# Performance work log

Measured on AMD Instinct MI355X. Metric: run time of the kernel, lower is better.

The kernel has to match this reference:

```python
import jax, jax.numpy as jnp
import numpy as np

B, T, D = 2, 2048, 2048
N, KH, H = 16, 8, 128  # query heads, kv heads, head_dim
S = 2048               # cache size
EPS = 1e-6
ROPE_THETA = 1000000.0
K_MASK = -0.7 * float(np.finfo(np.float32).max)  # jax _get_large_negative(float32)


def _rms_norm(x, w):
    rms = jnp.sqrt(jnp.mean(x.astype(jnp.float32) ** 2, axis=-1, keepdims=True) + EPS)
    return (w * x / rms).astype(x.dtype)


def _rope_embeddings(positions, head_dim):
    fraction = jnp.arange(0, head_dim, 2, dtype=jnp.float32) / head_dim
    inv_freq = 1.0 / (ROPE_THETA ** fraction)
    sinusoid = jnp.einsum('BT,k->BTk', positions.astype(jnp.float32), inv_freq,
                          precision=jax.lax.Precision.HIGHEST)
    return jnp.sin(sinusoid), jnp.cos(sinusoid)


def _apply_rope(x, sin, cos):
    h = x.shape[-1] // 2
    x1, x2 = x[..., :h], x[..., h:]
    s, c = sin[:, :, None, :], cos[:, :, None, :]
    return jnp.concatenate([x1 * c - x2 * s, x2 * c + x1 * s], axis=-1).astype(x.dtype)


def _positions_from_segment_ids(seg):
    t = seg.shape[1]
    pos = jnp.arange(t, dtype=jnp.int32)[None, :] - jnp.argmax(seg, axis=1)[:, None]
    return jnp.where(seg != 0, pos, 2 ** 30)


def _num_left_pad(seg):
    return jnp.sum(jnp.cumsum(seg != 0, axis=-1) == 0, axis=-1).astype(jnp.int32)


def _attention(x, q_w, k_w, v_w, o_w, q_norm_w, k_norm_w, k_cache, v_cache,
               segment_ids, start_ind, cur_ind):
    b, t, _ = x.shape
    s = k_cache.shape[1]
    n, kh, h = q_w.shape[1], k_w.shape[1], q_w.shape[2]

    q = _rms_norm(jnp.einsum('BTD,DNH->BTNH', x, q_w), q_norm_w)  # [B,T,N,H]
    k = _rms_norm(jnp.einsum('BSD,DKH->BSKH', x, k_w), k_norm_w)  # [B,T,K,H]
    v = jnp.einsum('BSD,DKH->BSKH', x, v_w)                       # [B,T,K,H]

    start = jnp.where(start_ind < 0, _num_left_pad(segment_ids), start_ind)
    pos = _positions_from_segment_ids(segment_ids) + cur_ind
    sin, cos = _rope_embeddings(pos, h)
    q = _apply_rope(q, sin, cos)
    k = _apply_rope(k, sin, cos)

    # KV-cache update at cur_ind
    k_cache = jax.lax.dynamic_update_slice(k_cache, k, (0, cur_ind, 0, 0))
    v_cache = jax.lax.dynamic_update_slice(v_cache, v, (0, cur_ind, 0, 0))

    # GQA: group query heads per kv head
    qg = q.reshape(b, t, kh, n // kh, h)
    logits = jnp.einsum('BTHGD,BSHD->BHGTS', qg, k_cache) * (h ** -0.5)

    q_pos = cur_ind + jnp.arange(t, dtype=jnp.int32)[None, :] - start[:, None]  # [B,T]
    ts = jnp.arange(s, dtype=jnp.int32)
    kv_seg = (ts[None, :] >= start[:, None]) & (ts[None, :] < cur_ind + t)      # [B,S] bool
    k_pos = ts[None, :] - start[:, None]                                        # [B,S]
    causal = k_pos[:, None, :] <= q_pos[:, :, None]                             # [B,T,S]
    # faithful to original: bool kv segment ids compared against int segment_ids
    seg_mask = kv_seg[:, None, :].astype(segment_ids.dtype) == segment_ids[:, :, None]
    final_mask = (causal & seg_mask)[:, None, None, :, :]                       # [B,1,1,T,S]

    logits = jnp.where(final_mask, logits, K_MASK)
    attn = jax.nn.softmax(logits.astype(jnp.float32), axis=-1).astype(logits.dtype)
    o = jnp.einsum('BHGTS,BSHD->BTHGD', attn, v_cache).reshape(b, t, n, h)
    return jnp.einsum('BTNH,NHD->BTD', o, o_w)


def setup_inputs() -> dict:
    key = jax.random.key(0)
    ks = jax.random.split(key, 5)
    scale = 0.02
    return {
        'x': jax.random.normal(ks[0], (B, T, D), jnp.float32),
        'q_w': jax.random.normal(ks[1], (D, N, H), jnp.float32) * scale,
        'k_w': jax.random.normal(ks[2], (D, KH, H), jnp.float32) * scale,
        'v_w': jax.random.normal(ks[3], (D, KH, H), jnp.float32) * scale,
        'o_w': jax.random.normal(ks[4], (N, H, D), jnp.float32) * scale,
        'q_norm_w': jnp.ones((H,), jnp.float32),
        'k_norm_w': jnp.ones((H,), jnp.float32),
        'k_cache': jnp.zeros((B, S, KH, H), jnp.float32),
        'v_cache': jnp.zeros((B, S, KH, H), jnp.float32),
        'segment_ids': jnp.ones((B, T), jnp.int32),
        'start_ind': jnp.zeros((B,), jnp.int32),
        'cur_ind': 0,
        'right_pads': 0,
    }


def reference(x, q_w, k_w, v_w, o_w, q_norm_w, k_norm_w, k_cache, v_cache,
              segment_ids, start_ind, cur_ind, right_pads):
    # right_pads only advances the cache write pointer (stateful side effect); it
    # does not affect the attention output.
    return _attention(x, q_w, k_w, v_w, o_w, q_norm_w, k_norm_w,
                      k_cache, v_cache, segment_ids, start_ind, cur_ind)
```

## Files before the change

kernel.cpp:

```cpp
#include <hip/hip_runtime.h>
#include <hip/hip_fp16.h>
#include <climits>
#include <math.h>

#define Bc   2
#define Tc   2048
#define Dc   2048
#define Nc   16
#define KHc  8
#define Hc   128
#define Sc   2048

constexpr float EPSc   = 1e-6f;
constexpr float SCALE2 = 0.1275174477984469f;

typedef short short8 __attribute__((ext_vector_type(8)));
typedef _Float16 half8 __attribute__((ext_vector_type(8)));
typedef __fp16 fp16x2 __attribute__((ext_vector_type(2)));
typedef float float4v __attribute__((ext_vector_type(4)));

union U16x8 { uint4 u; short8 s8; half8 h8; unsigned short us[8]; };
union H2U  { fp16x2 h; unsigned u; };
union S8H8 { short8 s; half8 h; };

__device__ __forceinline__ unsigned short f2bf(float f) {
    union { float f; unsigned u; } v; v.f = f;
    unsigned r = v.u + 0x7FFFu + ((v.u >> 16) & 1u);
    return (unsigned short)(r >> 16);
}
__device__ __forceinline__ float bf2f(unsigned short u) {
    union { unsigned u; float f; } v; v.u = ((unsigned)u) << 16;
    return v.f;
}

__device__ __forceinline__ void tc_body(const float* __restrict__ in,
                                        unsigned short* __restrict__ out,
                                        int R, int C, int bx, int by, int tid,
                                        float tile[32][33])
{
    int c0 = bx * 32, r0 = by * 32;
#pragma unroll
    for (int i = 0; i < 4; ++i) {
        int row = (tid >> 5) + i * 8, col = tid & 31;
        tile[row][col] = in[(size_t)(r0 + row) * C + c0 + col];
    }
    __syncthreads();
#pragma unroll
    for (int i = 0; i < 4; ++i) {
        int rowo = (tid >> 5) + i * 8, colo = tid & 31;
        out[(size_t)(c0 + rowo) * R + r0 + colo] = f2bf(tile[colo][rowo]);
    }
}

__global__ __launch_bounds__(256) void prep(const float* __restrict__ x,
                                            const float* __restrict__ qw,
                                            const float* __restrict__ kw,
                                            const float* __restrict__ vw,
                                            const float* __restrict__ ow,
                                            const int* __restrict__ seg,
                                            const int* __restrict__ start_ind,
                                            int* __restrict__ meta,
                                            unsigned short* __restrict__ xb,
                                            unsigned short* __restrict__ qkvwT,
                                            unsigned short* __restrict__ owT)
{
    __shared__ float tile[32][33];
    __shared__ int s_max, s_amax, s_nz;
    int id = blockIdx.x;
    int tid = threadIdx.x;

    if (id < Bc) {
        int b = id;
        if (tid == 0) { s_max = INT_MIN; s_amax = Tc; s_nz = Tc; }
        __syncthreads();
        int lmax = INT_MIN;
        for (int t = tid; t < Tc; t += 256) lmax = max(lmax, seg[b * Tc + t]);
        atomicMax(&s_max, lmax);
        __syncthreads();
        int mv = s_max;
        int lamax = Tc, lnz = Tc;
        for (int t = tid; t < Tc; t += 256) {
            int v = seg[b * Tc + t];
            if (v == mv) lamax = min(lamax, t);
            if (v != 0)  lnz   = min(lnz, t);
        }
        atomicMin(&s_amax, lamax);
        atomicMin(&s_nz, lnz);
        __syncthreads();
        if (tid == 0) {
            meta[b] = s_amax;
            int st = start_ind[b];
            meta[Bc + b] = (st < 0) ? s_nz : st;
        }
        return;
    }
    id -= Bc;
    if (id < 4096) {
        size_t base = ((size_t)id * 256 + tid) * 8;
        float4 a = *(const float4*)&x[base];
        float4 b = *(const float4*)&x[base + 4];
        U16x8 o;
        o.us[0] = f2bf(a.x); o.us[1] = f2bf(a.y); o.us[2] = f2bf(a.z); o.us[3] = f2bf(a.w);
        o.us[4] = f2bf(b.x); o.us[5] = f2bf(b.y); o.us[6] = f2bf(b.z); o.us[7] = f2bf(b.w);
        *(uint4*)&xb[base] = o.u;
        return;
    }
    id -= 4096;
    if (id < 4096) { tc_body(qw, qkvwT, 2048, 2048, id & 63, id >> 6, tid, tile); return; }
    id -= 4096;
    if (id < 2048) { tc_body(kw, qkvwT + (size_t)2048 * 2048, 2048, 1024, id & 31, id >> 5, tid, tile); return; }
    id -= 2048;
    if (id < 2048) { tc_body(vw, qkvwT + (size_t)3072 * 2048, 2048, 1024, id & 31, id >> 5, tid, tile); return; }
    id -= 2048;
    tc_body(ow, owT, 2048, 2048, id & 63, id >> 6, tid, tile);
}

#define GSYNC_IN()  do { asm volatile("" ::: "memory"); \
                         __builtin_amdgcn_s_barrier(); \
                         asm volatile("s_waitcnt lgkmcnt(0)" ::: "memory"); \
                         __builtin_amdgcn_sched_barrier(0); \
                         __builtin_amdgcn_s_setprio(1); } while (0)
#define GSYNC_OUT() do { __builtin_amdgcn_s_setprio(0); \
                         __builtin_amdgcn_sched_barrier(0); \
                         asm volatile("" ::: "memory"); \
                         __builtin_amdgcn_s_barrier(); } while (0)
#define GSYNC_OUT_KT() do { __builtin_amdgcn_s_setprio(0); \
                         __builtin_amdgcn_sched_barrier(0); \
                         asm volatile("s_waitcnt vmcnt(4)" ::: "memory"); \
                         __builtin_amdgcn_s_barrier(); \
                         asm volatile("" ::: "memory"); } while (0)

__global__ __launch_bounds__(512, 2) void gemm256(const unsigned short* __restrict__ A,
                                                  const unsigned short* __restrict__ BT,
                                                  void* __restrict__ Cout,
                                                  int M, int N, int K, int out_fp32)
{
    __shared__ __align__(16) unsigned short As[2 * 16384];
    __shared__ __align__(16) unsigned short Bs[2 * 16384];

    int tid = threadIdx.x;
    int lane = tid & 63, w = tid >> 6;
    int quad = lane >> 4, l15 = lane & 15;

    int gx = gridDim.x;
    int nwg = gx * gridDim.y;
    int lin = blockIdx.y * gx + blockIdx.x;
    int swz = (lin & 7) * (nwg >> 3) + (lin >> 3);
    int bm = (swz / gx) * 256, bn = (swz % gx) * 256;

    int KT = K >> 6;

    int colswz = (((lane & 7) ^ ((lane >> 3) & 7)) << 3);
    int r0 = (w * 2) * 8 + (lane >> 3);
    int r1 = (w * 2 + 1) * 8 + (lane >> 3);
    const unsigned short* Ab0 = A + (size_t)(bm + r0) * K + colswz;
    const unsigned short* Ab1 = A + (size_t)(bm + r1) * K + colswz;
    const unsigned short* Bb0 = BT + (size_t)(bn + r0) * K + colswz;
    const unsigned short* Bb1 = BT + (size_t)(bn + r1) * K + colswz;
    size_t hK = (size_t)128 * K;

    unsigned short* dA0 = As + (w * 2) * 512;
    unsigned short* dA1 = As + (w * 2 + 1) * 512;
    unsigned short* dB0 = Bs + (w * 2) * 512;
    unsigned short* dB1 = Bs + (w * 2 + 1) * 512;

    auto stA = [&](int kt, int h, int bufp) __attribute__((always_inline)) {
        __builtin_amdgcn_global_load_lds(
            (__attribute__((address_space(1))) void*)(Ab0 + h * hK + (size_t)kt * 64),
            (__attribute__((address_space(3))) void*)(dA0 + bufp * 16384 + h * 8192), 16, 0, 0);
        __builtin_amdgcn_global_load_lds(
            (__attribute__((address_space(1))) void*)(Ab1 + h * hK + (size_t)kt * 64),
            (__attribute__((address_space(3))) void*)(dA1 + bufp * 16384 + h * 8192), 16, 0, 0);
    };
    auto stB = [&](int kt, int h, int bufp) __attribute__((always_inline)) {
        __builtin_amdgcn_global_load_lds(
            (__attribute__((address_space(1))) void*)(Bb0 + h * hK + (size_t)kt * 64),
            (__attribute__((address_space(3))) void*)(dB0 + bufp * 16384 + h * 8192), 16, 0, 0);
        __builtin_amdgcn_global_load_lds(
            (__attribute__((address_space(1))) void*)(Bb1 + h * hK + (size_t)kt * 64),
            (__attribute__((address_space(3))) void*)(dB1 + bufp * 16384 + h * 8192), 16, 0, 0);
    };

    int ards = (w >> 2) * 8192;
    int brds = (w & 3) * 4096;
    int rowb = l15 * 64;
    int swA = l15 & 7;
    int cof0 = ((quad) ^ swA) << 3;
    int cof1 = ((4 + quad) ^ swA) << 3;

    float4v acc[8][4];
#pragma unroll
    for (int i = 0; i < 8; ++i)
#pragma unroll
        for (int j = 0; j < 4; ++j) acc[i][j] = (float4v)0.f;

    stA(0, 0, 0); stA(0, 1, 0); stB(0, 0, 0); stB(0, 1, 0);
    stA(1, 0, 1); stA(1, 1, 1);
    asm volatile("s_waitcnt vmcnt(4)" ::: "memory");
    __builtin_amdgcn_s_barrier();
    asm volatile("" ::: "memory");

    auto ktile = [&](int kt, int bufp) __attribute__((always_inline)) {
        bool sB = (kt + 1) < KT;
        bool sA = (kt + 2) < KT;
        const unsigned short* ab = As + bufp * 16384 + ards + rowb;
        const unsigned short* bb = Bs + bufp * 16384 + brds + rowb;
        short8 afl[2][4], afh[2][4], bfa[2][2], bfb[2][2];

#pragma unroll
        for (int mi = 0; mi < 4; ++mi) {
            afl[0][mi] = *(const short8*)&ab[mi * 1024 + cof0];
            afl[1][mi] = *(const short8*)&ab[mi * 1024 + cof1];
        }
#pragma unroll
        for (int ni = 0; ni < 2; ++ni) {
            bfa[0][ni] = *(const short8*)&bb[ni * 1024 + cof0];
            bfa[1][ni] = *(const short8*)&bb[ni * 1024 + cof1];
        }
        if (sB) stB(kt + 1, 0, bufp ^ 1);
        GSYNC_IN();
#pragma unroll
        for (int kk = 0; kk < 2; ++kk)
#pragma unroll
            for (int mi = 0; mi < 4; ++mi)
#pragma unroll
                for (int ni = 0; ni < 2; ++ni)
                    acc[mi][ni] = __builtin_amdgcn_mfma_f32_16x16x32_bf16(afl[kk][mi], bfa[kk][ni], acc[mi][ni], 0, 0, 0);
        GSYNC_OUT();

#pragma unroll
        for (int mi = 0; mi < 4; ++mi) {
            afh[0][mi] = *(const short8*)&ab[(4 + mi) * 1024 + cof0];
            afh[1][mi] = *(const short8*)&ab[(4 + mi) * 1024 + cof1];
        }
#pragma unroll
        for (int ni = 0; ni < 2; ++ni) {
            bfb[0][ni] = *(const short8*)&bb[(2 + ni) * 1024 + cof0];
            bfb[1][ni] = *(const short8*)&bb[(2 + ni) * 1024 + cof1];
        }
        if (sB) stB(kt + 1, 1, bufp ^ 1);
        GSYNC_IN();
#pragma unroll
        for (int kk = 0; kk < 2; ++kk)
#pragma unroll
            for (int mi = 0; mi < 4; ++mi)
#pragma unroll
                for (int ni = 0; ni < 2; ++ni)
                    acc[mi][2 + ni] = __builtin_amdgcn_mfma_f32_16x16x32_bf16(afl[kk][mi], bfb[kk][ni], acc[mi][2 + ni], 0, 0, 0);
        GSYNC_OUT();

#pragma unroll
        for (int ni = 0; ni < 2; ++ni) {
            bfa[0][ni] = *(const short8*)&bb[ni * 1024 + cof0];
            bfa[1][ni] = *(const short8*)&bb[ni * 1024 + cof1];
        }
        if (sA) stA(kt + 2, 0, bufp);
        GSYNC_IN();
#pragma unroll
        for (int kk = 0; kk < 2; ++kk)
#pragma unroll
            for (int mi = 0; mi < 4; ++mi)
#pragma unroll
                for (int ni = 0; ni < 2; ++ni)
                    acc[4 + mi][ni] = __builtin_amdgcn_mfma_f32_16x16x32_bf16(afh[kk][mi], bfa[kk][ni], acc[4 + mi][ni], 0, 0, 0);
        GSYNC_OUT();

#pragma unroll
        for (int ni = 0; ni < 2; ++ni) {
            bfb[0][ni] = *(const short8*)&bb[(2 + ni) * 1024 + cof0];
            bfb[1][ni] = *(const short8*)&bb[(2 + ni) * 1024 + cof1];
        }
        if (sA) stA(kt + 2, 1, bufp);
        GSYNC_IN();
#pragma unroll
        for (int kk = 0; kk < 2; ++kk)
#pragma unroll
            for (int mi = 0; mi < 4; ++mi)
#pragma unroll
                for (int ni = 0; ni < 2; ++ni)
                    acc[4 + mi][2 + ni] = __builtin_amdgcn_mfma_f32_16x16x32_bf16(afh[kk][mi], bfb[kk][ni], acc[4 + mi][2 + ni], 0, 0, 0);
        GSYNC_OUT_KT();
    };

    for (int kt = 0; kt < KT; kt += 2) {
        ktile(kt, 0);
        ktile(kt + 1, 1);
    }

    int wm = (w >> 2) * 128, wn = (w & 3) * 64;
#pragma unroll
    for (int mi = 0; mi < 8; ++mi)
#pragma unroll
        for (int ni = 0; ni < 4; ++ni)
#pragma unroll
            for (int reg = 0; reg < 4; ++reg) {
                int row = bm + wm + mi * 16 + quad * 4 + reg;
                int col = bn + wn + ni * 16 + l15;
                float v = acc[mi][ni][reg];
                if (out_fp32) ((float*)Cout)[(size_t)row * N + col] = v;
                else ((unsigned short*)Cout)[(size_t)row * N + col] = f2bf(v);
            }
}

__global__ __launch_bounds__(256) void post(unsigned short* __restrict__ QKVh,
                                            unsigned short* __restrict__ Kall,
                                            unsigned short* __restrict__ Vt,
                                            const float* __restrict__ qw,
                                            const float* __restrict__ kw,
                                            const int* __restrict__ seg,
                                            const int* __restrict__ meta,
                                            const int* __restrict__ cur_ptr,
                                            const float* __restrict__ kc,
                                            const float* __restrict__ vc)
{
    int id = blockIdx.x;
    int tid = threadIdx.x;
    int cur = cur_ptr[0];

    if (id < 24576) {
        int rowid = id * 4 + (tid >> 6);
        int lane = tid & 63;
        int hh = rowid % 24;
        int bt = rowid / 24;
        int t = bt & (Tc - 1);
        int b = bt >> 11;

        const unsigned short* in;
        unsigned short* out;
        const float* wt;
        if (hh < 16) {
            unsigned short* p = QKVh + (size_t)bt * 4096 + hh * Hc;
            in = p; out = p; wt = qw;
        } else {
            int kh = hh - 16;
            in = QKVh + (size_t)bt * 4096 + 2048 + kh * Hc;
            out = Kall + (((size_t)b * Sc + cur + t) * KHc + kh) * Hc;
            wt = kw;
        }
        float v1 = bf2f(in[lane]), v2 = bf2f(in[lane + 64]);
        float ssq = v1 * v1 + v2 * v2;
#pragma unroll
        for (int off = 1; off < 64; off <<= 1) ssq += __shfl_xor(ssq, off);
        float rinv = rsqrtf(ssq * (1.0f / Hc) + EPSc);

        int sg = seg[bt];
        long long pos = (sg != 0) ? (long long)(t - meta[b]) : (long long)(1 << 30);
        float posf = (float)(pos + (long long)cur);
        float inv_freq = exp2f(-(float)lane * (19.931568569324174f / 64.0f));
        float s, c;
        sincosf(posf * inv_freq, &s, &c);

        float n1 = wt[lane] * v1 * rinv;
        float n2 = wt[lane + 64] * v2 * rinv;
        out[lane]      = f2bf(n1 * c - n2 * s);
        out[lane + 64] = f2bf(n2 * c + n1 * s);
        return;
    }
    id -= 24576;
    if (id < 2048) {
        size_t base = ((size_t)id * 256 + tid) * 8;
        int s = (int)((base >> 10) & (Sc - 1));
        if (s >= cur && s < cur + Tc) return;
        float4 a = *(const float4*)&kc[base];
        float4 b = *(const float4*)&kc[base + 4];
        U16x8 o;
        o.us[0] = f2bf(a.x); o.us[1] = f2bf(a.y); o.us[2] = f2bf(a.z); o.us[3] = f2bf(a.w);
        o.us[4] = f2bf(b.x); o.us[5] = f2bf(b.y); o.us[6] = f2bf(b.z); o.us[7] = f2bf(b.w);
        *(uint4*)&Kall[base] = o.u;
        return;
    }
    id -= 2048;
    {
        int gid = id * 256 + tid;
        int h  = gid & 127;
        int s8 = ((gid >> 7) & 255) * 8;
        int kh = (gid >> 15) & 7;
        int b  = gid >> 18;
        int curT = cur + Tc;
        unsigned short tmp[8];
#pragma unroll
        for (int e = 0; e < 8; ++e) {
            int s = s8 + e;
            float f;
            if (s >= cur && s < curT)
                f = bf2f(QKVh[(size_t)(b * Tc + (s - cur)) * 4096 + 3072 + kh * Hc + h]);
            else
                f = vc[((size_t)(b * Sc + s) * KHc + kh) * Hc + h];
            tmp[e] = __half_as_ushort(__float2half(f));
        }
        *(uint4*)&Vt[(((size_t)b * KHc + kh) * Hc + h) * Sc + s8] = *(uint4*)tmp;
    }
}

__global__ __launch_bounds__(512, 4) void flash_mfma(const unsigned short* __restrict__ Qb,
                                                     const unsigned short* __restrict__ Kall,
                                                     const unsigned short* __restrict__ Vt,
                                                     const int* __restrict__ seg,
                                                     const int* __restrict__ meta,
                                                     const int* __restrict__ cur_ptr,
                                                     unsigned short* __restrict__ Ob)
{
    __shared__ __align__(16) unsigned short Ks[64 * 128];
    __shared__ __align__(16) unsigned short Vs[128 * 64];
    __shared__ __align__(16) unsigned short Ps[128 * 64];

    int tid = threadIdx.x;
    int lane = tid & 63, w = tid >> 6;
    int quad = lane >> 4, l15 = lane & 15;
    int bid = blockIdx.x;
    int raw = bid & 15;
    int n  = (bid >> 4) & 15;
    int b  = bid >> 8;
    int qt = (b == 0) ? raw : (15 - raw);
    int kh = n >> 1;
    int cur = cur_ptr[0];
    int startb = meta[Bc + b];
    int curT = cur + Tc;
    int t0 = qt * 128 + w * 16;

    short8 qf[4];
#pragma unroll
    for (int ks = 0; ks < 4; ++ks) {
        int row = t0 + l15;
        U16x8 uq;
        uq.u = *(const uint4*)&Qb[(size_t)(b * Tc + row) * 4096 + n * Hc + ks * 32 + quad * 8];
        qf[ks] = uq.s8;
    }

    int trow0 = t0 + l15;
    int sg0 = seg[b * Tc + trow0];
    int cls = (sg0 == 0) ? 0 : ((sg0 == 1) ? 1 : 2);
    int ct  = cur + trow0;
    unsigned long long mball = __ballot(cls == 1);
    bool allseg1 = (mball == 0xFFFFFFFFFFFFFFFFull);

    float lsum = 0.f;
    float4v oT[8];
#pragma unroll
    for (int i = 0; i < 8; ++i) oT[i] = (float4v)0.f;

    int s_end = min(Sc, cur + qt * 128 + 128);
    int nch = (s_end + 63) >> 6;

    const size_t kstride = (size_t)KHc * Hc;
    const unsigned short* kptr[2];
    unsigned short* kdst[2];
#pragma unroll
    for (int i = 0; i < 2; ++i) {
        int j = w * 2 + i;
        int row = j * 4 + (lane >> 4);
        int pl = lane & 15;
        int pg = pl ^ ((row >> 1) & 7);
        kptr[i] = Kall + (size_t)b * Sc * kstride + (size_t)row * kstride + kh * Hc + pg * 8;
        kdst[i] = Ks + j * 512;
    }
    const unsigned short* vptr[2];
    unsigned short* vdst[2];
#pragma unroll
    for (int i = 0; i < 2; ++i) {
        int j = w * 2 + i;
        int h = j * 8 + (lane >> 3);
        int pl = lane & 7;
        int pg = pl ^ ((h >> 1) & 7);
        vptr[i] = Vt + ((size_t)b * KHc + kh) * (size_t)Hc * Sc + (size_t)h * Sc + pg * 8;
        vdst[i] = Vs + j * 512;
    }
    int sw3 = (l15 >> 1) & 7;
    int sw8 = l15 & 7;
    unsigned short* psrow = Ps + (w * 16 + l15) * 64;

    for (int c = 0; c < nch; ++c) {
        int s0 = c * 64;
#pragma unroll
        for (int i = 0; i < 2; ++i) {
            __builtin_amdgcn_global_load_lds(
                (__attribute__((address_space(1))) void*)(kptr[i] + (size_t)s0 * kstride),
                (__attribute__((address_space(3))) void*)kdst[i], 16, 0, 0);
            __builtin_amdgcn_global_load_lds(
                (__attribute__((address_space(1))) void*)(vptr[i] + s0),
                (__attribute__((address_space(3))) void*)vdst[i], 16, 0, 0);
        }
        __syncthreads();

        float4v st[4];
#pragma unroll
        for (int i = 0; i < 4; ++i) st[i] = (float4v)0.f;
        __builtin_amdgcn_s_setprio(1);
#pragma unroll
        for (int ks = 0; ks < 4; ++ks) {
#pragma unroll
            for (int stile = 0; stile < 4; ++stile) {
                short8 kf = *(const short8*)&Ks[(stile * 16 + l15) * 128 + ((ks * 4 + quad) ^ sw3) * 8];
                st[stile] = __builtin_amdgcn_mfma_f32_16x16x32_bf16(kf, qf[ks], st[stile], 0, 0, 0);
            }
        }
        __builtin_amdgcn_s_setprio(0);

        bool fullok = allseg1 && (s0 >= startb) && (s0 + 63 <= cur + t0) && (s0 + 63 < curT);

#pragma unroll
        for (int stile = 0; stile < 4; ++stile) {
            float p0, p1, p2, p3;
            if (fullok) {
                p0 = exp2f(st[stile][0] * SCALE2);
                p1 = exp2f(st[stile][1] * SCALE2);
                p2 = exp2f(st[stile][2] * SCALE2);
                p3 = exp2f(st[stile][3] * SCALE2);
            } else {
                float pp[4];
#pragma unroll
                for (int reg = 0; reg < 4; ++reg) {
                    int s = s0 + stile * 16 + quad * 4 + reg;
                    int kvseg = (s >= startb && s < curT) ? 1 : 0;
                    bool ok = (s <= ct) && (cls == kvseg);
                    pp[reg] = exp2f(ok ? st[stile][reg] * SCALE2 : -1e30f);
                }
                p0 = pp[0]; p1 = pp[1]; p2 = pp[2]; p3 = pp[3];
            }
            lsum += (p0 + p1) + (p2 + p3);
            H2U a, d;
            a.h = __builtin_amdgcn_cvt_pkrtz(p0, p1);
            d.h = __builtin_amdgcn_cvt_pkrtz(p2, p3);
            uint2 pk; pk.x = a.u; pk.y = d.u;
            *(uint2*)&psrow[(((stile * 2 + (quad >> 1)) ^ sw8) << 3) + (quad & 1) * 4] = pk;
        }

        __builtin_amdgcn_s_setprio(1);
#pragma unroll
        for (int kk = 0; kk < 2; ++kk) {
            S8H8 pf;
            pf.s = *(const short8*)&psrow[((kk * 4 + quad) ^ sw8) << 3];
#pragma unroll
            for (int htile = 0; htile < 8; ++htile) {
                S8H8 vf;
                vf.s = *(const short8*)&Vs[(htile * 16 + l15) * 64 + ((kk * 4 + quad) ^ sw3) * 8];
                oT[htile] = __builtin_amdgcn_mfma_f32_16x16x32_f16(vf.h, pf.h, oT[htile], 0, 0, 0);
            }
        }
        __builtin_amdgcn_s_setprio(0);

        __syncthreads();
    }

    float l = lsum;
    l += __shfl_xor(l, 16);
    l += __shfl_xor(l, 32);
    float linv = (l > 0.f) ? (1.0f / l) : 0.f;

    {
        int trow = t0 + l15;
        size_t base = ((size_t)(b * Tc + trow) * Nc + n) * Hc;
#pragma unroll
        for (int htile = 0; htile < 8; ++htile) {
            float4v v = oT[htile];
            unsigned short r0 = f2bf(v[0] * linv);
            unsigned short r1 = f2bf(v[1] * linv);
            unsigned short r2 = f2bf(v[2] * linv);
            unsigned short r3 = f2bf(v[3] * linv);
            uint2 pk;
            pk.x = (unsigned)r0 | ((unsigned)r1 << 16);
            pk.y = (unsigned)r2 | ((unsigned)r3 << 16);
            *(uint2*)&Ob[base + htile * 16 + quad * 4] = pk;
        }
    }
}

extern "C" void kernel_launch(void* const* d_in, const int* in_sizes, int n_in,
                              void* d_out, int out_size, void* d_ws, size_t ws_size,
                              hipStream_t stream)
{
    const float* x        = (const float*)d_in[0];
    const float* q_w      = (const float*)d_in[1];
    const float* k_w      = (const float*)d_in[2];
    const float* v_w      = (const float*)d_in[3];
    const float* o_w      = (const float*)d_in[4];
    const float* q_norm_w = (const float*)d_in[5];
    const float* k_norm_w = (const float*)d_in[6];
    const float* k_cache  = (const float*)d_in[7];
    const float* v_cache  = (const float*)d_in[8];
    const int*   seg      = (const int*)d_in[9];
    const int*   startind = (const int*)d_in[10];
    const int*   cur_ptr  = (const int*)d_in[11];
    (void)in_sizes; (void)n_in; (void)out_size; (void)ws_size;

    char* base = (char*)d_ws;
    int* meta = (int*)base;
    unsigned short* QKVh = (unsigned short*)(base + 1024);
    unsigned short* Kall = (unsigned short*)(base + 33555456);
    unsigned short* Vt   = (unsigned short*)(base + 41944064);
    unsigned short* xb   = (unsigned short*)(base + 50332672);
    unsigned short* qkvwT= (unsigned short*)(base + 67109888);
    unsigned short* owT  = (unsigned short*)(base + 83887104);
    unsigned short* Ob   = xb;

    prep<<<Bc + 4096 + 4096 + 2048 + 2048 + 4096, 256, 0, stream>>>(
        x, q_w, k_w, v_w, o_w, seg, startind, meta, xb, qkvwT, owT);

    gemm256<<<dim3(16, 16), 512, 0, stream>>>(xb, qkvwT, QKVh, Bc * Tc, 4096, Dc, 0);

    post<<<24576 + 2048 + 2048, 256, 0, stream>>>(QKVh, Kall, Vt,
        q_norm_w, k_norm_w, seg, meta, cur_ptr, k_cache, v_cache);

    flash_mfma<<<Bc * Nc * (Tc / 128), 512, 0, stream>>>(QKVh, Kall, Vt, seg, meta, cur_ptr, Ob);

    gemm256<<<dim3(8, 16), 512, 0, stream>>>(Ob, owT, d_out, Bc * Tc, Dc, Nc * Hc, 1);
}
```

Measured before the change: 393.0 us.

## Restructure GEMM k-loop to two barriers per tile with prefetch two ahead

Replaces the four-phase ping-pong schedule, which had a barrier pair around each MFMA quarter, with a two-phase loop. All A and B fragments are read from LDS up front, and half the MFMAs run before a single barrier. Global loads for tile kt+2 are then issued into the just-freed buffer and overlap the remaining MFMAs, with a vmcnt wait and barrier at the end. This removes barrier and sync overhead per k-tile but raises register pressure from holding all fragments at once and changes the load/compute interleaving.

```diff
diff --git a/kernel.cpp b/kernel.cpp
--- a/kernel.cpp
+++ b/kernel.cpp
@@ -115,21 +115,6 @@
     tc_body(ow, owT, 2048, 2048, id & 63, id >> 6, tid, tile);
 }
 
-#define GSYNC_IN()  do { asm volatile("" ::: "memory"); \
-                         __builtin_amdgcn_s_barrier(); \
-                         asm volatile("s_waitcnt lgkmcnt(0)" ::: "memory"); \
-                         __builtin_amdgcn_sched_barrier(0); \
-                         __builtin_amdgcn_s_setprio(1); } while (0)
-#define GSYNC_OUT() do { __builtin_amdgcn_s_setprio(0); \
-                         __builtin_amdgcn_sched_barrier(0); \
-                         asm volatile("" ::: "memory"); \
-                         __builtin_amdgcn_s_barrier(); } while (0)
-#define GSYNC_OUT_KT() do { __builtin_amdgcn_s_setprio(0); \
-                         __builtin_amdgcn_sched_barrier(0); \
-                         asm volatile("s_waitcnt vmcnt(4)" ::: "memory"); \
-                         __builtin_amdgcn_s_barrier(); \
-                         asm volatile("" ::: "memory"); } while (0)
-
 __global__ __launch_bounds__(512, 2) void gemm256(const unsigned short* __restrict__ A,
                                                   const unsigned short* __restrict__ BT,
                                                   void* __restrict__ Cout,
@@ -195,14 +180,12 @@
         for (int j = 0; j < 4; ++j) acc[i][j] = (float4v)0.f;
 
     stA(0, 0, 0); stA(0, 1, 0); stB(0, 0, 0); stB(0, 1, 0);
-    stA(1, 0, 1); stA(1, 1, 1);
-    asm volatile("s_waitcnt vmcnt(4)" ::: "memory");
+    stA(1, 0, 1); stA(1, 1, 1); stB(1, 0, 1); stB(1, 1, 1);
+    asm volatile("s_waitcnt vmcnt(8)" ::: "memory");
     __builtin_amdgcn_s_barrier();
     asm volatile("" ::: "memory");
 
     auto ktile = [&](int kt, int bufp) __attribute__((always_inline)) {
-        bool sB = (kt + 1) < KT;
-        bool sA = (kt + 2) < KT;
         const unsigned short* ab = As + bufp * 16384 + ards + rowb;
         const unsigned short* bb = Bs + bufp * 16384 + brds + rowb;
         short8 afl[2][4], afh[2][4], bfa[2][2], bfb[2][2];
@@ -217,29 +200,24 @@
             bfa[0][ni] = *(const short8*)&bb[ni * 1024 + cof0];
             bfa[1][ni] = *(const short8*)&bb[ni * 1024 + cof1];
         }
-        if (sB) stB(kt + 1, 0, bufp ^ 1);
-        GSYNC_IN();
-#pragma unroll
-        for (int kk = 0; kk < 2; ++kk)
-#pragma unroll
-            for (int mi = 0; mi < 4; ++mi)
-#pragma unroll
-                for (int ni = 0; ni < 2; ++ni)
-                    acc[mi][ni] = __builtin_amdgcn_mfma_f32_16x16x32_bf16(afl[kk][mi], bfa[kk][ni], acc[mi][ni], 0, 0, 0);
-        GSYNC_OUT();
-
+#pragma unroll
+        for (int ni = 0; ni < 2; ++ni) {
+            bfb[0][ni] = *(const short8*)&bb[(2 + ni) * 1024 + cof0];
+            bfb[1][ni] = *(const short8*)&bb[(2 + ni) * 1024 + cof1];
+        }
 #pragma unroll
         for (int mi = 0; mi < 4; ++mi) {
             afh[0][mi] = *(const short8*)&ab[(4 + mi) * 1024 + cof0];
             afh[1][mi] = *(const short8*)&ab[(4 + mi) * 1024 + cof1];
         }
-#pragma unroll
-        for (int ni = 0; ni < 2; ++ni) {
-            bfb[0][ni] = *(const short8*)&bb[(2 + ni) * 1024 + cof0];
-            bfb[1][ni] = *(const short8*)&bb[(2 + ni) * 1024 + cof1];
-        }
-        if (sB) stB(kt + 1, 1, bufp ^ 1);
-        GSYNC_IN();
+        __builtin_amdgcn_s_setprio(1);
+#pragma unroll
+        for (int kk = 0; kk < 2; ++kk)
+#pragma unroll
+            for (int mi = 0; mi < 4; ++mi)
+#pragma unroll
+                for (int ni = 0; ni < 2; ++ni)
+                    acc[mi][ni] = __builtin_amdgcn_mfma_f32_16x16x32_bf16(afl[kk][mi], bfa[kk][ni], acc[mi][ni], 0, 0, 0);
 #pragma unroll
         for (int kk = 0; kk < 2; ++kk)
 #pragma unroll
@@ -247,15 +225,18 @@
 #pragma unroll
                 for (int ni = 0; ni < 2; ++ni)
                     acc[mi][2 + ni] = __builtin_amdgcn_mfma_f32_16x16x32_bf16(afl[kk][mi], bfb[kk][ni], acc[mi][2 + ni], 0, 0, 0);
-        GSYNC_OUT();
-
-#pragma unroll
-        for (int ni = 0; ni < 2; ++ni) {
-            bfa[0][ni] = *(const short8*)&bb[ni * 1024 + cof0];
-            bfa[1][ni] = *(const short8*)&bb[ni * 1024 + cof1];
-        }
-        if (sA) stA(kt + 2, 0, bufp);
-        GSYNC_IN();
+        __builtin_amdgcn_s_setprio(0);
+        asm volatile("s_waitcnt lgkmcnt(0)" ::: "memory");
+        __builtin_amdgcn_sched_barrier(0);
+        __builtin_amdgcn_s_barrier();
+        asm volatile("" ::: "memory");
+
+        bool sA = (kt + 2) < KT;
+        if (sA) {
+            stA(kt + 2, 0, bufp); stA(kt + 2, 1, bufp);
+            stB(kt + 2, 0, bufp); stB(kt + 2, 1, bufp);
+        }
+        __builtin_amdgcn_s_setprio(1);
 #pragma unroll
         for (int kk = 0; kk < 2; ++kk)
 #pragma unroll
@@ -263,15 +244,6 @@
 #pragma unroll
                 for (int ni = 0; ni < 2; ++ni)
                     acc[4 + mi][ni] = __builtin_amdgcn_mfma_f32_16x16x32_bf16(afh[kk][mi], bfa[kk][ni], acc[4 + mi][ni], 0, 0, 0);
-        GSYNC_OUT();
-
-#pragma unroll
-        for (int ni = 0; ni < 2; ++ni) {
-            bfb[0][ni] = *(const short8*)&bb[(2 + ni) * 1024 + cof0];
-            bfb[1][ni] = *(const short8*)&bb[(2 + ni) * 1024 + cof1];
-        }
-        if (sA) stA(kt + 2, 1, bufp);
-        GSYNC_IN();
 #pragma unroll
         for (int kk = 0; kk < 2; ++kk)
 #pragma unroll
@@ -279,7 +251,12 @@
 #pragma unroll
                 for (int ni = 0; ni < 2; ++ni)
                     acc[4 + mi][2 + ni] = __builtin_amdgcn_mfma_f32_16x16x32_bf16(afh[kk][mi], bfb[kk][ni], acc[4 + mi][2 + ni], 0, 0, 0);
-        GSYNC_OUT_KT();
+        __builtin_amdgcn_s_setprio(0);
+        if (sA) asm volatile("s_waitcnt vmcnt(8)" ::: "memory");
+        else    asm volatile("s_waitcnt vmcnt(0)" ::: "memory");
+        __builtin_amdgcn_sched_barrier(0);
+        __builtin_amdgcn_s_barrier();
+        asm volatile("" ::: "memory");
     };
 
     for (int kt = 0; kt < KT; kt += 2) {
```

New measurement: 457.8 us. 1.16x slower.

## Add 128x128 tiled GEMM for output projection and vectorize weight transpose

Applied to the files above, without the earlier changes.

Adds a new gemm128 kernel (256 threads, 128x128 tiles, double-buffered LDS via global_load_lds) and uses it for the output projection. The previous 256x256 tiling launched only 128 workgroups, and the smaller tile raises that to 512 so more of the GPU's compute units stay busy. The prep transpose is also changed to use float4 loads and 16-byte packed bf16 stores, cutting the number of memory transactions. The trade-off is lower data reuse per tile and more total global traffic for the GEMM.

```diff
diff --git a/kernel.cpp b/kernel.cpp
--- a/kernel.cpp
+++ b/kernel.cpp
@@ -39,16 +39,21 @@
                                         float tile[32][33])
 {
     int c0 = bx * 32, r0 = by * 32;
-#pragma unroll
-    for (int i = 0; i < 4; ++i) {
-        int row = (tid >> 5) + i * 8, col = tid & 31;
-        tile[row][col] = in[(size_t)(r0 + row) * C + c0 + col];
+    {
+        int row = tid >> 3, col = (tid & 7) * 4;
+        float4 v = *(const float4*)&in[(size_t)(r0 + row) * C + c0 + col];
+        tile[row][col]     = v.x;
+        tile[row][col + 1] = v.y;
+        tile[row][col + 2] = v.z;
+        tile[row][col + 3] = v.w;
     }
     __syncthreads();
-#pragma unroll
-    for (int i = 0; i < 4; ++i) {
-        int rowo = (tid >> 5) + i * 8, colo = tid & 31;
-        out[(size_t)(c0 + rowo) * R + r0 + colo] = f2bf(tile[colo][rowo]);
+    if (tid < 128) {
+        int rowo = tid >> 2, s8 = (tid & 3) * 8;
+        U16x8 o;
+#pragma unroll
+        for (int k = 0; k < 8; ++k) o.us[k] = f2bf(tile[s8 + k][rowo]);
+        *(uint4*)&out[(size_t)(c0 + rowo) * R + r0 + s8] = o.u;
     }
 }
 
@@ -290,6 +295,136 @@
     int wm = (w >> 2) * 128, wn = (w & 3) * 64;
 #pragma unroll
     for (int mi = 0; mi < 8; ++mi)
+#pragma unroll
+        for (int ni = 0; ni < 4; ++ni)
+#pragma unroll
+            for (int reg = 0; reg < 4; ++reg) {
+                int row = bm + wm + mi * 16 + quad * 4 + reg;
+                int col = bn + wn + ni * 16 + l15;
+                float v = acc[mi][ni][reg];
+                if (out_fp32) ((float*)Cout)[(size_t)row * N + col] = v;
+                else ((unsigned short*)Cout)[(size_t)row * N + col] = f2bf(v);
+            }
+}
+
+__global__ __launch_bounds__(256, 2) void gemm128(const unsigned short* __restrict__ A,
+                                                  const unsigned short* __restrict__ BT,
+                                                  void* __restrict__ Cout,
+                                                  int M, int N, int K, int out_fp32)
+{
+    __shared__ __align__(16) unsigned short As[2 * 8192];
+    __shared__ __align__(16) unsigned short Bs[2 * 8192];
+
+    int tid = threadIdx.x;
+    int lane = tid & 63, w = tid >> 6;
+    int quad = lane >> 4, l15 = lane & 15;
+
+    int gx = gridDim.x;
+    int nwg = gx * gridDim.y;
+    int lin = blockIdx.y * gx + blockIdx.x;
+    int swz = (lin & 7) * (nwg >> 3) + (lin >> 3);
+    int bm = (swz / gx) * 128, bn = (swz % gx) * 128;
+
+    int KT = K >> 6;
+
+    int colswz = (((lane & 7) ^ ((lane >> 3) & 7)) << 3);
+    int r0 = w * 32 + (lane >> 3);
+    const unsigned short* Ab = A + (size_t)(bm + r0) * K + colswz;
+    const unsigned short* Bb = BT + (size_t)(bn + r0) * K + colswz;
+    size_t rowK8 = (size_t)8 * K;
+
+    unsigned short* dA = As + w * 2048;
+    unsigned short* dB = Bs + w * 2048;
+
+    auto stA = [&](int kt, int bufp) __attribute__((always_inline)) {
+#pragma unroll
+        for (int i = 0; i < 4; ++i)
+            __builtin_amdgcn_global_load_lds(
+                (__attribute__((address_space(1))) void*)(Ab + (size_t)i * rowK8 + (size_t)kt * 64),
+                (__attribute__((address_space(3))) void*)(dA + bufp * 8192 + i * 512), 16, 0, 0);
+    };
+    auto stB = [&](int kt, int bufp) __attribute__((always_inline)) {
+#pragma unroll
+        for (int i = 0; i < 4; ++i)
+            __builtin_amdgcn_global_load_lds(
+                (__attribute__((address_space(1))) void*)(Bb + (size_t)i * rowK8 + (size_t)kt * 64),
+                (__attribute__((address_space(3))) void*)(dB + bufp * 8192 + i * 512), 16, 0, 0);
+    };
+
+    int wm = (w >> 1) * 64, wn = (w & 1) * 64;
+    int swk = l15 & 7;
+    int cof0 = ((quad) ^ swk) << 3;
+    int cof1 = ((4 + quad) ^ swk) << 3;
+    const int arow = (wm + l15) * 64;
+    const int brow = (wn + l15) * 64;
+
+    float4v acc[4][4];
+#pragma unroll
+    for (int i = 0; i < 4; ++i)
+#pragma unroll
+        for (int j = 0; j < 4; ++j) acc[i][j] = (float4v)0.f;
+
+    stA(0, 0); stB(0, 0);
+    stA(1, 1);
+    asm volatile("s_waitcnt vmcnt(4)" ::: "memory");
+    __builtin_amdgcn_s_barrier();
+    asm volatile("" ::: "memory");
+
+    auto ktile = [&](int kt, int bufp) __attribute__((always_inline)) {
+        const unsigned short* ab = As + bufp * 8192 + arow;
+        const unsigned short* bb = Bs + bufp * 8192 + brow;
+        short8 af[2][4], bf[2][4];
+
+        if (kt + 1 < KT) stB(kt + 1, bufp ^ 1);
+#pragma unroll
+        for (int mi = 0; mi < 4; ++mi) {
+            af[0][mi] = *(const short8*)&ab[mi * 1024 + cof0];
+            af[1][mi] = *(const short8*)&ab[mi * 1024 + cof1];
+        }
+#pragma unroll
+        for (int ni = 0; ni < 4; ++ni) {
+            bf[0][ni] = *(const short8*)&bb[ni * 1024 + cof0];
+            bf[1][ni] = *(const short8*)&bb[ni * 1024 + cof1];
+        }
+        __builtin_amdgcn_s_setprio(1);
+#pragma unroll
+        for (int kk = 0; kk < 2; ++kk)
+#pragma unroll
+            for (int mi = 0; mi < 4; ++mi)
+#pragma unroll
+                for (int ni = 0; ni < 2; ++ni)
+                    acc[mi][ni] = __builtin_amdgcn_mfma_f32_16x16x32_bf16(af[kk][mi], bf[kk][ni], acc[mi][ni], 0, 0, 0);
+        __builtin_amdgcn_s_setprio(0);
+        asm volatile("s_waitcnt lgkmcnt(0)" ::: "memory");
+        __builtin_amdgcn_sched_barrier(0);
+        __builtin_amdgcn_s_barrier();
+        asm volatile("" ::: "memory");
+
+        bool sA = (kt + 2) < KT;
+        if (sA) stA(kt + 2, bufp);
+        __builtin_amdgcn_s_setprio(1);
+#pragma unroll
+        for (int kk = 0; kk < 2; ++kk)
+#pragma unroll
+            for (int mi = 0; mi < 4; ++mi)
+#pragma unroll
+                for (int ni = 2; ni < 4; ++ni)
+                    acc[mi][ni] = __builtin_amdgcn_mfma_f32_16x16x32_bf16(af[kk][mi], bf[kk][ni], acc[mi][ni], 0, 0, 0);
+        __builtin_amdgcn_s_setprio(0);
+        if (sA) asm volatile("s_waitcnt vmcnt(4)" ::: "memory");
+        else    asm volatile("s_waitcnt vmcnt(0)" ::: "memory");
+        __builtin_amdgcn_sched_barrier(0);
+        __builtin_amdgcn_s_barrier();
+        asm volatile("" ::: "memory");
+    };
+
+    for (int kt = 0; kt < KT; kt += 2) {
+        ktile(kt, 0);
+        ktile(kt + 1, 1);
+    }
+
+#pragma unroll
+    for (int mi = 0; mi < 4; ++mi)
 #pragma unroll
         for (int ni = 0; ni < 4; ++ni)
 #pragma unroll
@@ -603,5 +738,5 @@
 
     flash_mfma<<<Bc * Nc * (Tc / 128), 512, 0, stream>>>(QKVh, Kall, Vt, seg, meta, cur_ptr, Ob);
 
-    gemm256<<<dim3(8, 16), 512, 0, stream>>>(Ob, owT, d_out, Bc * Tc, Dc, Nc * Hc, 1);
-}
+    gemm128<<<dim3(16, 32), 256, 0, stream>>>(Ob, owT, d_out, Bc * Tc, Dc, Nc * Hc, 1);
+}
```

Result: faster. 369.3 us (-6.1%).
